# Kernel tuning notes

Measured on AMD Instinct MI355X. Metric: run time of the kernel, lower is better.

Reference implementation:

```python
import jax, jax.numpy as jnp
import numpy as np

NEG_SLOPE = 0.2  # LeakyReLU slope
B, F_BAND, T = 32, 128, 2048
HID, NCLASS = 256, 64


def _corrcoef(m):
    # m: [..., n, k] -> correlation matrix between rows, [..., n, n] (torch.corrcoef semantics)
    m = m - m.mean(axis=-1, keepdims=True)
    c = jnp.einsum('...ik,...jk->...ij', m, m)
    d = jnp.sqrt(jnp.clip(jnp.diagonal(c, axis1=-2, axis2=-1), 0.0, None))
    corr = c / (d[..., :, None] * d[..., None, :])
    return jnp.clip(corr, -1.0, 1.0)


def _leaky(x):
    return jnp.where(x >= 0, x, NEG_SLOPE * x)


def setup_inputs() -> dict:
    key = jax.random.key(0)
    ks = jax.random.split(key, 9)
    def lin(k, fin, fout):
        return jax.random.normal(k, (fin, fout), dtype=jnp.float32) / np.sqrt(fin)
    x = jax.random.normal(ks[0], (B, F_BAND, T), dtype=jnp.float32)
    return {
        'x': x,
        'W1': lin(ks[1], T, HID),      'b1': jnp.zeros((HID,), jnp.float32),
        'W2': lin(ks[2], HID, HID),    'b2': jnp.zeros((HID,), jnp.float32),
        'W3': lin(ks[3], HID, NCLASS), 'b3': jnp.zeros((NCLASS,), jnp.float32),
        'W4': lin(ks[4], NCLASS, NCLASS), 'b4': jnp.zeros((NCLASS,), jnp.float32),
    }


def reference(x, W1, b1, W2, b2, W3, b3, W4, b4):
    Bs, Fb, Tt = x.shape
    node = Fb
    step = node  # typeFeature=2 -> overlap=0
    A = len(range(0, Tt - node, step))  # number of time windows
    # windows: x[:, :, a*node:(a+1)*node] -> [B, A, F, node]
    xw = x[:, :, :A * node].reshape(Bs, Fb, A, node).transpose(0, 2, 1, 3)
    # torch.corrcoef(fi.T): rows = window-column index (node), variables over F bands
    adj = _corrcoef(jnp.swapaxes(xw, -1, -2))  # [B, A, node, node] == [B, A, F, F]
    adj = jnp.nan_to_num((adj + 1.0) * 0.5)
    # gnnBlock vectorized over all A windows (x broadcast along A). Dropout is eval-mode no-op.
    h = _leaky(jnp.einsum('banm,bmt->bant', adj, x) @ W1 + b1)    # [B,A,F,HID]
    h = _leaky(jnp.einsum('banm,bamh->banh', adj, h) @ W2 + b2)   # [B,A,F,HID]
    xa = _leaky(jnp.einsum('banm,bamh->banh', adj, h) @ W3 + b3)  # [B,A,F,C]
    # typeFeature==2 head: mean over nodes, corrcoef over windows, gc4
    xa = xa.mean(axis=2)         # [B, A, C]
    adj2 = _corrcoef(xa)         # [B, A, A]
    out = _leaky(jnp.einsum('bij,bjc->bic', adj2, xa) @ W4 + b4)  # [B, A, C]
    # max over dim=1; GradMultiply with grad_mul=1.0 is identity in fwd
    return out.max(axis=1)       # [B, C]
```

## Files before the change

### kernel.cpp

```cpp
#include <hip/hip_runtime.h>


typedef float f32x4 __attribute__((ext_vector_type(4)));
typedef __bf16 bf16x8 __attribute__((ext_vector_type(8)));
typedef unsigned short u16x8 __attribute__((ext_vector_type(8)));

__device__ inline unsigned short f2b(float f) {
  unsigned int u = __float_as_uint(f);
  unsigned int r = u + 0x7fffu + ((u >> 16) & 1u);
  return (unsigned short)(r >> 16);
}
__device__ inline float leaky(float v) { return v >= 0.f ? v : 0.2f * v; }

#define SWZ(k, r) ((k) ^ (((r) & 7) << 3))

__global__ __launch_bounds__(256) void k_prepw(const float* __restrict__ W1,
                                               const float* __restrict__ W2,
                                               const float* __restrict__ W3,
                                               unsigned short* __restrict__ W1T,
                                               unsigned short* __restrict__ W2T,
                                               unsigned short* __restrict__ W3T) {
  __shared__ float t[64][65];
  const int bid = blockIdx.x;
  const int tid = threadIdx.x;
  const float* src;
  unsigned short* dst;
  int K, N, k0, n0;
  if (bid < 128) {
    src = W1; dst = W1T; K = 2048; N = 256;
    k0 = (bid >> 2) * 64; n0 = (bid & 3) * 64;
  } else if (bid < 144) {
    src = W2; dst = W2T; K = 256; N = 256;
    int i = bid - 128; k0 = (i >> 2) * 64; n0 = (i & 3) * 64;
  } else {
    src = W3; dst = W3T; K = 256; N = 64;
    int i = bid - 144; k0 = i * 64; n0 = 0;
  }
#pragma unroll
  for (int it = 0; it < 16; ++it) {
    int e = tid + it * 256, r = e >> 6, c = e & 63;
    t[r][c] = src[(size_t)(k0 + r) * N + n0 + c];
  }
  __syncthreads();
#pragma unroll
  for (int it = 0; it < 16; ++it) {
    int e = tid + it * 256, rr = e >> 6, cc = e & 63;
    dst[(size_t)(n0 + rr) * K + k0 + cc] = f2b(t[cc][rr]);
  }
}

__global__ __launch_bounds__(512) void k_front(const float* __restrict__ x,
                                               const unsigned short* __restrict__ W1T,
                                               unsigned short* __restrict__ xT,
                                               unsigned short* __restrict__ XW1T) {
  __shared__ __align__(16) char ldsbuf[16896];
  const int bid = blockIdx.x;
  const int tid = threadIdx.x;
  if (bid >= 64) {
    float (*t)[65] = reinterpret_cast<float (*)[65]>(ldsbuf);
    int i = bid - 64;
    int b = i >> 6, rem = i & 63;
    int t0 = (rem >> 1) * 64, f0 = (rem & 1) * 64;
    const float* xb = x + ((size_t)b * 128 + f0) * 2048 + t0;
    int r = tid >> 3, c8 = (tid & 7) * 8;
    f32x4 v0 = *(const f32x4*)&xb[(size_t)r * 2048 + c8];
    f32x4 v1 = *(const f32x4*)&xb[(size_t)r * 2048 + c8 + 4];
    *(f32x4*)&t[r][c8] = v0;
    *(f32x4*)&t[r][c8 + 4] = v1;
    __syncthreads();
    u16x8 s;
#pragma unroll
    for (int q = 0; q < 8; ++q) s[q] = f2b(t[c8 + q][r]);
    *(u16x8*)&xT[((size_t)b * 2048 + t0 + r) * 128 + f0 + c8] = s;
  } else {
    unsigned short (*sX)[64 * 64] = reinterpret_cast<unsigned short (*)[64 * 64]>(ldsbuf);
    const int b = bid >> 1, f0 = (bid & 1) * 64;
    const int w = tid >> 6, lane = tid & 63;
    const int l15 = lane & 15, l4 = lane >> 4;
    const float* xb = x + ((size_t)b * 128 + f0) * 2048;
    const int fr = tid >> 3, k8 = (tid & 7) * 8;
    f32x4 xr0, xr1;
    f32x4 acc[2][4] = {};

    auto LOADX = [&](int kb) {
      xr0 = *(const f32x4*)&xb[(size_t)fr * 2048 + kb * 64 + k8];
      xr1 = *(const f32x4*)&xb[(size_t)fr * 2048 + kb * 64 + k8 + 4];
    };
    auto STOREX = [&](int buf) {
      u16x8 s;
#pragma unroll
      for (int q = 0; q < 8; ++q) s[q] = f2b(q < 4 ? xr0[q] : xr1[q - 4]);
      *(u16x8*)&sX[buf][fr * 64 + SWZ(k8, fr)] = s;
    };

    LOADX(0);
    STOREX(0);
    __syncthreads();
    for (int kb = 0; kb < 32; ++kb) {
      if (kb < 31) LOADX(kb + 1);
      const int buf = kb & 1;
#pragma unroll
      for (int ks = 0; ks < 2; ++ks) {
        bf16x8 af[2];
#pragma unroll
        for (int mt = 0; mt < 2; ++mt)
          af[mt] = *(const bf16x8*)&W1T[(size_t)(w * 32 + mt * 16 + l15) * 2048 + kb * 64 + ks * 32 + l4 * 8];
#pragma unroll
        for (int nt = 0; nt < 4; ++nt) {
          int br = nt * 16 + l15;
          bf16x8 bf = *(const bf16x8*)&sX[buf][br * 64 + SWZ(ks * 32 + l4 * 8, br)];
#pragma unroll
          for (int mt = 0; mt < 2; ++mt)
            acc[mt][nt] = __builtin_amdgcn_mfma_f32_16x16x32_bf16(af[mt], bf, acc[mt][nt], 0, 0, 0);
        }
      }
      if (kb < 31) {
        STOREX(buf ^ 1);
        __syncthreads();
      }
    }
#pragma unroll
    for (int mt = 0; mt < 2; ++mt)
#pragma unroll
      for (int nt = 0; nt < 4; ++nt)
#pragma unroll
        for (int r = 0; r < 4; ++r) {
          int p = w * 32 + mt * 16 + l4 * 4 + r;
          XW1T[((size_t)b * 256 + p) * 128 + f0 + nt * 16 + l15] = f2b(acc[mt][nt][r]);
        }
  }
}

__global__ __launch_bounds__(512) void k_chain(
    const unsigned short* __restrict__ xT, const unsigned short* __restrict__ XW1T,
    const unsigned short* __restrict__ W2T, const unsigned short* __restrict__ W3T,
    const float* __restrict__ b1g, const float* __restrict__ b2g,
    const float* __restrict__ b3g, float* __restrict__ gXa) {
  __shared__ __align__(16) unsigned short R0[128 * 128];
  __shared__ __align__(16) unsigned short R1[128 * 128];
  __shared__ float fS[256];

  const int tid = threadIdx.x;
  const int w = tid >> 6, lane = tid & 63;
  const int l15 = lane & 15, l4 = lane >> 4;
  const int ridx = (blockIdx.x & 7) * 60 + (blockIdx.x >> 3);
  const int b = ridx / 15, a = ridx % 15;
  const int m0 = w * 16;
  const unsigned short* XWb = XW1T + (size_t)b * 256 * 128;
  const float inv128 = 1.f / 128.f;

  const unsigned short* src = xT + ((size_t)b * 2048 + (size_t)a * 128) * 128;
#pragma unroll 1
  for (int it = 0; it < 4; ++it) {
    int tt = tid + it * 512;
    int j = tt >> 4, f8 = (tt & 15) * 8;
    *(u16x8*)&R1[j * 128 + SWZ(f8, j)] = *(const u16x8*)&src[j * 128 + f8];
  }
  __syncthreads();

  bf16x8 afw[4];
#pragma unroll
  for (int ks = 0; ks < 4; ++ks) {
    int ar = m0 + l15;
    afw[ks] = *(const bf16x8*)&R1[ar * 128 + SWZ(ks * 32 + l4 * 8, ar)];
  }
  bf16x8 ones;
#pragma unroll
  for (int q = 0; q < 8; ++q) ones[q] = (__bf16)1.0f;
  f32x4 sacc = {}, dacc = {};
#pragma unroll
  for (int ks = 0; ks < 4; ++ks) {
    sacc = __builtin_amdgcn_mfma_f32_16x16x32_bf16(afw[ks], ones, sacc, 0, 0, 0);
    dacc = __builtin_amdgcn_mfma_f32_16x16x32_bf16(afw[ks], afw[ks], dacc, 0, 0, 0);
  }
#pragma unroll
  for (int r = 0; r < 4; ++r) {
    if (l15 == 0) fS[m0 + l4 * 4 + r] = sacc[r];
    if (l15 == l4 * 4 + r)
      fS[128 + m0 + l4 * 4 + r] = dacc[r] - sacc[r] * sacc[r] * inv128;
  }
  __syncthreads();

  float div[4];
#pragma unroll
  for (int r = 0; r < 4; ++r) {
    float d = fS[128 + m0 + l4 * 4 + r];
    div[r] = d > 0.f ? __frsqrt_rn(d) : 0.f;
  }
#pragma unroll 1
  for (int nt = 0; nt < 8; ++nt) {
    int col = nt * 16 + l15;
    f32x4 c = {};
#pragma unroll
    for (int ks = 0; ks < 4; ++ks) {
      bf16x8 bf = *(const bf16x8*)&R1[col * 128 + SWZ(ks * 32 + l4 * 8, col)];
      c = __builtin_amdgcn_mfma_f32_16x16x32_bf16(afw[ks], bf, c, 0, 0, 0);
    }
    float fc = fS[col];
    float dc = fS[128 + col];
    float djv = dc > 0.f ? __frsqrt_rn(dc) : 0.f;
#pragma unroll
    for (int r = 0; r < 4; ++r) {
      float v = (c[r] - sacc[r] * fc * inv128) * div[r] * djv;
      v = fminf(1.f, fmaxf(-1.f, v));
      v = 0.5f * v + 0.5f;
      if (div[r] == 0.f || djv == 0.f) v = 0.f;
      int row = m0 + l4 * 4 + r;
      R0[row * 128 + SWZ(col, row)] = f2b(v);
    }
  }
  bf16x8 afj[4];
#pragma unroll
  for (int ks = 0; ks < 4; ++ks)
    afj[ks] = *(const bf16x8*)&R0[(m0 + l15) * 128 + SWZ(ks * 32 + l4 * 8, m0 + l15)];
  __syncthreads();

#pragma unroll 1
  for (int half = 0; half < 2; ++half) {
    unsigned short* Rd = half ? R0 : R1;
#pragma unroll 1
    for (int nt = 0; nt < 8; ++nt) {
      f32x4 acc = {};
      const unsigned short* Bp = &XWb[(size_t)(half * 128 + nt * 16 + l15) * 128 + l4 * 8];
#pragma unroll
      for (int ks = 0; ks < 4; ++ks) {
        bf16x8 bf = *(const bf16x8*)&Bp[ks * 32];
        acc = __builtin_amdgcn_mfma_f32_16x16x32_bf16(afj[ks], bf, acc, 0, 0, 0);
      }
      float bias = b1g[half * 128 + nt * 16 + l15];
#pragma unroll
      for (int r = 0; r < 4; ++r) {
        int row = m0 + l4 * 4 + r;
        Rd[row * 128 + SWZ(nt * 16 + l15, row)] = f2b(leaky(acc[r] + bias));
      }
    }
  }
  __syncthreads();

  f32x4 u2[2][8] = {};
  {
#pragma unroll
    for (int ks = 0; ks < 8; ++ks) {
      bf16x8 a0 = *(const bf16x8*)&W2T[(size_t)(w * 32 + l15) * 256 + ks * 32 + l4 * 8];
      bf16x8 a1 = *(const bf16x8*)&W2T[(size_t)(w * 32 + 16 + l15) * 256 + ks * 32 + l4 * 8];
      const unsigned short* Rs = (ks < 4) ? R1 : R0;
      int kk = (ks & 3) * 32 + l4 * 8;
#pragma unroll
      for (int nt = 0; nt < 8; ++nt) {
        int br = nt * 16 + l15;
        bf16x8 bf = *(const bf16x8*)&Rs[br * 128 + SWZ(kk, br)];
        u2[0][nt] = __builtin_amdgcn_mfma_f32_16x16x32_bf16(a0, bf, u2[0][nt], 0, 0, 0);
        u2[1][nt] = __builtin_amdgcn_mfma_f32_16x16x32_bf16(a1, bf, u2[1][nt], 0, 0, 0);
      }
    }
  }
  __syncthreads();

#pragma unroll
  for (int mt = 0; mt < 2; ++mt)
#pragma unroll
    for (int nt = 0; nt < 8; ++nt)
#pragma unroll
      for (int r = 0; r < 4; ++r) {
        int grow = w * 32 + mt * 16 + l4 * 4 + r;
        int col = nt * 16 + l15;
        unsigned short* Rd = (grow < 128) ? R0 : R1;
        int lr = grow & 127;
        Rd[lr * 128 + SWZ(col, lr)] = f2b(u2[mt][nt][r]);
      }
  __syncthreads();

  f32x4 h2acc[16];
#pragma unroll
  for (int nt = 0; nt < 16; ++nt) h2acc[nt] = f32x4{0.f, 0.f, 0.f, 0.f};
#pragma unroll
  for (int ks = 0; ks < 4; ++ks)
#pragma unroll
    for (int nt = 0; nt < 16; ++nt) {
      int brl = (nt & 7) * 16 + l15;
      const unsigned short* Rs = (nt < 8) ? R0 : R1;
      bf16x8 bf = *(const bf16x8*)&Rs[brl * 128 + SWZ(ks * 32 + l4 * 8, brl)];
      h2acc[nt] = __builtin_amdgcn_mfma_f32_16x16x32_bf16(afj[ks], bf, h2acc[nt], 0, 0, 0);
    }
  __syncthreads();

#pragma unroll
  for (int nt = 0; nt < 16; ++nt) {
    float bias = b2g[nt * 16 + l15];
#pragma unroll
    for (int r = 0; r < 4; ++r) {
      int row = m0 + l4 * 4 + r;
      int coll = (nt & 7) * 16 + l15;
      unsigned short* Rd = (nt < 8) ? R0 : R1;
      Rd[row * 128 + SWZ(coll, row)] = f2b(leaky(h2acc[nt][r] + bias));
    }
  }
  __syncthreads();

  f32x4 u3[4] = {};
  const int mrow = (w >> 1) * 16, ntb = (w & 1) * 4;
#pragma unroll
  for (int kh = 0; kh < 2; ++kh) {
    const unsigned short* Rs = kh ? R1 : R0;
#pragma unroll
    for (int ks = 0; ks < 4; ++ks) {
      bf16x8 a3 = *(const bf16x8*)&W3T[(size_t)(mrow + l15) * 256 + kh * 128 + ks * 32 + l4 * 8];
#pragma unroll
      for (int nti = 0; nti < 4; ++nti) {
        int br = (ntb + nti) * 16 + l15;
        bf16x8 bf = *(const bf16x8*)&Rs[br * 128 + SWZ(ks * 32 + l4 * 8, br)];
        u3[nti] = __builtin_amdgcn_mfma_f32_16x16x32_bf16(a3, bf, u3[nti], 0, 0, 0);
      }
    }
  }
  __syncthreads();

#pragma unroll
  for (int nti = 0; nti < 4; ++nti)
#pragma unroll
    for (int r = 0; r < 4; ++r) {
      int grow = mrow + l4 * 4 + r;
      int col = (ntb + nti) * 16 + l15;
      R0[grow * 128 + SWZ(col, grow)] = f2b(u3[nti][r]);
    }
  __syncthreads();

  {
    float* pf = reinterpret_cast<float*>(R1);
#pragma unroll 1
    for (int nt = 0; nt < 4; ++nt) {
      f32x4 acc = {};
      int br = nt * 16 + l15;
#pragma unroll
      for (int ks = 0; ks < 4; ++ks) {
        bf16x8 bf = *(const bf16x8*)&R0[br * 128 + SWZ(ks * 32 + l4 * 8, br)];
        acc = __builtin_amdgcn_mfma_f32_16x16x32_bf16(afj[ks], bf, acc, 0, 0, 0);
      }
      float bias = b3g[br];
      float v = 0.f;
#pragma unroll
      for (int r = 0; r < 4; ++r) v += leaky(acc[r] + bias);
      v += __shfl_xor(v, 16);
      v += __shfl_xor(v, 32);
      if (l4 == 0) pf[w * 64 + br] = v;
    }
  }
  __syncthreads();
  if (tid < 64) {
    const float* pf = reinterpret_cast<const float*>(R1);
    float s = 0.f;
#pragma unroll
    for (int gg = 0; gg < 8; ++gg) s += pf[gg * 64 + tid];
    gXa[((size_t)b * 15 + a) * 64 + tid] = s * (1.f / 128.f);
  }
}

__global__ __launch_bounds__(256) void k_head(const float* __restrict__ gXa,
                                              const float* __restrict__ W4,
                                              const float* __restrict__ b4,
                                              float* __restrict__ out) {
  __shared__ float xb[15 * 64];
  __shared__ float c2[15 * 16];
  __shared__ float mu[15];
  __shared__ float dinv[15];
  __shared__ float yy[15 * 64];
  __shared__ float zz[15 * 64];
  const int b = blockIdx.x;
  const int tid = threadIdx.x;
  for (int e = tid; e < 960; e += 256) xb[e] = gXa[(size_t)b * 960 + e];
  __syncthreads();
  if (tid < 15) {
    float s = 0.f;
    for (int c = 0; c < 64; ++c) s += xb[tid * 64 + c];
    mu[tid] = s * (1.f / 64.f);
  }
  __syncthreads();
  if (tid < 225) {
    int p = tid / 15, q = tid % 15;
    float s = 0.f;
    for (int c = 0; c < 64; ++c)
      s += (xb[p * 64 + c] - mu[p]) * (xb[q * 64 + c] - mu[q]);
    c2[p * 16 + q] = s;
  }
  __syncthreads();
  if (tid < 15) {
    float d = c2[tid * 16 + tid];
    dinv[tid] = d > 0.f ? (1.f / sqrtf(d)) : 0.f;
  }
  __syncthreads();
  if (tid < 225) {
    int p = tid / 15, q = tid % 15;
    float v = c2[p * 16 + q] * dinv[p] * dinv[q];
    v = fminf(1.f, fmaxf(-1.f, v));
    if (dinv[p] == 0.f || dinv[q] == 0.f) v = 0.f;
    c2[p * 16 + q] = v;
  }
  __syncthreads();
  for (int e = tid; e < 960; e += 256) {
    int p = e >> 6, c = e & 63;
    float s = 0.f;
    for (int q = 0; q < 15; ++q) s += c2[p * 16 + q] * xb[q * 64 + c];
    yy[e] = s;
  }
  __syncthreads();
  for (int e = tid; e < 960; e += 256) {
    int p = e >> 6, c = e & 63;
    float s = b4[c];
    for (int k = 0; k < 64; ++k) s += yy[p * 64 + k] * W4[k * 64 + c];
    zz[e] = leaky(s);
  }
  __syncthreads();
  if (tid < 64) {
    float m = -INFINITY;
    for (int p = 0; p < 15; ++p) m = fmaxf(m, zz[p * 64 + tid]);
    out[(size_t)b * 64 + tid] = m;
  }
}

extern "C" void kernel_launch(void* const* d_in, const int* in_sizes, int n_in,
                              void* d_out, int out_size, void* d_ws, size_t ws_size,
                              hipStream_t stream) {
  const float* x  = (const float*)d_in[0];
  const float* W1 = (const float*)d_in[1];
  const float* b1 = (const float*)d_in[2];
  const float* W2 = (const float*)d_in[3];
  const float* b2 = (const float*)d_in[4];
  const float* W3 = (const float*)d_in[5];
  const float* b3 = (const float*)d_in[6];
  const float* W4 = (const float*)d_in[7];
  const float* b4 = (const float*)d_in[8];
  float* out = (float*)d_out;

  char* ws = (char*)d_ws;
  unsigned short* xT   = (unsigned short*)ws;
  unsigned short* XW1T = (unsigned short*)(ws + 16777216);
  unsigned short* W1T  = (unsigned short*)(ws + 18874368);
  unsigned short* W2T  = (unsigned short*)(ws + 19922944);
  unsigned short* W3T  = (unsigned short*)(ws + 20054016);
  float* gXa           = (float*)(ws + 20086784);

  k_prepw<<<148, 256, 0, stream>>>(W1, W2, W3, W1T, W2T, W3T);
  k_front<<<2112, 512, 0, stream>>>(x, W1T, xT, XW1T);
  k_chain<<<480, 512, 0, stream>>>(xT, XW1T, W2T, W3T, b1, b2, b3, gXa);
  k_head<<<32, 256, 0, stream>>>(gXa, W4, b4, out);
}
```

Baseline: 131.3 us.

## Move x transpose into weight prep kernel, split XW1 GEMM, prefetch operands in chain

The x-to-bf16 transpose now runs inside the weight-prep kernel instead of sharing a launch with the x·W1 GEMM, and that GEMM becomes its own 64-block kernel. In k_chain, global loads of the XW1 B tiles, W2 A fragments and W3 fragments are software-prefetched one iteration ahead or hoisted before a barrier, to hide global memory latency. The split gives the 64 GEMM blocks a launch with no competition from the transpose blocks, but that launch underfills the GPU. The transpose now uses 256-thread blocks with smaller 4-element stores, and the prefetching adds register pressure.

Result: slower. 139.7 us (+6.4%).

```diff
diff --git a/kernel.cpp b/kernel.cpp
--- a/kernel.cpp
+++ b/kernel.cpp
@@ -3,6 +3,7 @@
 
 typedef float f32x4 __attribute__((ext_vector_type(4)));
 typedef __bf16 bf16x8 __attribute__((ext_vector_type(8)));
+typedef unsigned short u16x4 __attribute__((ext_vector_type(4)));
 typedef unsigned short u16x8 __attribute__((ext_vector_type(8)));
 
 __device__ inline unsigned short f2b(float f) {
@@ -14,121 +15,126 @@
 
 #define SWZ(k, r) ((k) ^ (((r) & 7) << 3))
 
-__global__ __launch_bounds__(256) void k_prepw(const float* __restrict__ W1,
-                                               const float* __restrict__ W2,
-                                               const float* __restrict__ W3,
-                                               unsigned short* __restrict__ W1T,
-                                               unsigned short* __restrict__ W2T,
-                                               unsigned short* __restrict__ W3T) {
+__global__ __launch_bounds__(256) void k_prep(const float* __restrict__ x,
+                                              const float* __restrict__ W1,
+                                              const float* __restrict__ W2,
+                                              const float* __restrict__ W3,
+                                              unsigned short* __restrict__ W1T,
+                                              unsigned short* __restrict__ W2T,
+                                              unsigned short* __restrict__ W3T,
+                                              unsigned short* __restrict__ xT) {
   __shared__ float t[64][65];
   const int bid = blockIdx.x;
   const int tid = threadIdx.x;
-  const float* src;
-  unsigned short* dst;
-  int K, N, k0, n0;
-  if (bid < 128) {
-    src = W1; dst = W1T; K = 2048; N = 256;
-    k0 = (bid >> 2) * 64; n0 = (bid & 3) * 64;
-  } else if (bid < 144) {
-    src = W2; dst = W2T; K = 256; N = 256;
-    int i = bid - 128; k0 = (i >> 2) * 64; n0 = (i & 3) * 64;
+  if (bid < 148) {
+    const float* src;
+    unsigned short* dst;
+    int K, N, k0, n0;
+    if (bid < 128) {
+      src = W1; dst = W1T; K = 2048; N = 256;
+      k0 = (bid >> 2) * 64; n0 = (bid & 3) * 64;
+    } else if (bid < 144) {
+      src = W2; dst = W2T; K = 256; N = 256;
+      int i = bid - 128; k0 = (i >> 2) * 64; n0 = (i & 3) * 64;
+    } else {
+      src = W3; dst = W3T; K = 256; N = 64;
+      int i = bid - 144; k0 = i * 64; n0 = 0;
+    }
+#pragma unroll
+    for (int it = 0; it < 16; ++it) {
+      int e = tid + it * 256, r = e >> 6, c = e & 63;
+      t[r][c] = src[(size_t)(k0 + r) * N + n0 + c];
+    }
+    __syncthreads();
+#pragma unroll
+    for (int it = 0; it < 16; ++it) {
+      int e = tid + it * 256, rr = e >> 6, cc = e & 63;
+      dst[(size_t)(n0 + rr) * K + k0 + cc] = f2b(t[cc][rr]);
+    }
   } else {
-    src = W3; dst = W3T; K = 256; N = 64;
-    int i = bid - 144; k0 = i * 64; n0 = 0;
-  }
-#pragma unroll
-  for (int it = 0; it < 16; ++it) {
-    int e = tid + it * 256, r = e >> 6, c = e & 63;
-    t[r][c] = src[(size_t)(k0 + r) * N + n0 + c];
-  }
-  __syncthreads();
-#pragma unroll
-  for (int it = 0; it < 16; ++it) {
-    int e = tid + it * 256, rr = e >> 6, cc = e & 63;
-    dst[(size_t)(n0 + rr) * K + k0 + cc] = f2b(t[cc][rr]);
-  }
-}
-
-__global__ __launch_bounds__(512) void k_front(const float* __restrict__ x,
-                                               const unsigned short* __restrict__ W1T,
-                                               unsigned short* __restrict__ xT,
-                                               unsigned short* __restrict__ XW1T) {
-  __shared__ __align__(16) char ldsbuf[16896];
+    int idx = bid - 148;
+    int b = idx >> 6, rem = idx & 63;
+    int tt = rem >> 1, ft = rem & 1;
+    int t0 = tt * 64, f0 = ft * 64;
+    const float* xb = x + ((size_t)b * 128 + f0) * 2048 + t0;
+#pragma unroll
+    for (int it = 0; it < 16; ++it) {
+      int e = tid + it * 256, r = e >> 6, c = e & 63;
+      t[r][c] = xb[(size_t)r * 2048 + c];
+    }
+    __syncthreads();
+    unsigned short* dst = xT + ((size_t)b * 2048 + t0) * 128 + f0;
+#pragma unroll
+    for (int it = 0; it < 4; ++it) {
+      int e = tid + it * 256, rr = e >> 4, c4 = (e & 15) * 4;
+      u16x4 s;
+#pragma unroll
+      for (int q = 0; q < 4; ++q) s[q] = f2b(t[c4 + q][rr]);
+      *(u16x4*)&dst[rr * 128 + c4] = s;
+    }
+  }
+}
+
+__global__ __launch_bounds__(512) void k_xw1(const float* __restrict__ x,
+                                             const unsigned short* __restrict__ W1T,
+                                             unsigned short* __restrict__ XW1T) {
+  __shared__ __align__(16) unsigned short sX[2][64 * 64];
   const int bid = blockIdx.x;
   const int tid = threadIdx.x;
-  if (bid >= 64) {
-    float (*t)[65] = reinterpret_cast<float (*)[65]>(ldsbuf);
-    int i = bid - 64;
-    int b = i >> 6, rem = i & 63;
-    int t0 = (rem >> 1) * 64, f0 = (rem & 1) * 64;
-    const float* xb = x + ((size_t)b * 128 + f0) * 2048 + t0;
-    int r = tid >> 3, c8 = (tid & 7) * 8;
-    f32x4 v0 = *(const f32x4*)&xb[(size_t)r * 2048 + c8];
-    f32x4 v1 = *(const f32x4*)&xb[(size_t)r * 2048 + c8 + 4];
-    *(f32x4*)&t[r][c8] = v0;
-    *(f32x4*)&t[r][c8 + 4] = v1;
-    __syncthreads();
+  const int b = bid >> 1, f0 = (bid & 1) * 64;
+  const int w = tid >> 6, lane = tid & 63;
+  const int l15 = lane & 15, l4 = lane >> 4;
+  const float* xb = x + ((size_t)b * 128 + f0) * 2048;
+  const int fr = tid >> 3, k8 = (tid & 7) * 8;
+  f32x4 xr0, xr1;
+  f32x4 acc[2][4] = {};
+
+  auto LOADX = [&](int kb) {
+    xr0 = *(const f32x4*)&xb[(size_t)fr * 2048 + kb * 64 + k8];
+    xr1 = *(const f32x4*)&xb[(size_t)fr * 2048 + kb * 64 + k8 + 4];
+  };
+  auto STOREX = [&](int buf) {
     u16x8 s;
 #pragma unroll
-    for (int q = 0; q < 8; ++q) s[q] = f2b(t[c8 + q][r]);
-    *(u16x8*)&xT[((size_t)b * 2048 + t0 + r) * 128 + f0 + c8] = s;
-  } else {
-    unsigned short (*sX)[64 * 64] = reinterpret_cast<unsigned short (*)[64 * 64]>(ldsbuf);
-    const int b = bid >> 1, f0 = (bid & 1) * 64;
-    const int w = tid >> 6, lane = tid & 63;
-    const int l15 = lane & 15, l4 = lane >> 4;
-    const float* xb = x + ((size_t)b * 128 + f0) * 2048;
-    const int fr = tid >> 3, k8 = (tid & 7) * 8;
-    f32x4 xr0, xr1;
-    f32x4 acc[2][4] = {};
-
-    auto LOADX = [&](int kb) {
-      xr0 = *(const f32x4*)&xb[(size_t)fr * 2048 + kb * 64 + k8];
-      xr1 = *(const f32x4*)&xb[(size_t)fr * 2048 + kb * 64 + k8 + 4];
-    };
-    auto STOREX = [&](int buf) {
-      u16x8 s;
-#pragma unroll
-      for (int q = 0; q < 8; ++q) s[q] = f2b(q < 4 ? xr0[q] : xr1[q - 4]);
-      *(u16x8*)&sX[buf][fr * 64 + SWZ(k8, fr)] = s;
-    };
-
-    LOADX(0);
-    STOREX(0);
-    __syncthreads();
-    for (int kb = 0; kb < 32; ++kb) {
-      if (kb < 31) LOADX(kb + 1);
-      const int buf = kb & 1;
-#pragma unroll
-      for (int ks = 0; ks < 2; ++ks) {
-        bf16x8 af[2];
+    for (int q = 0; q < 8; ++q) s[q] = f2b(q < 4 ? xr0[q] : xr1[q - 4]);
+    *(u16x8*)&sX[buf][fr * 64 + SWZ(k8, fr)] = s;
+  };
+
+  LOADX(0);
+  STOREX(0);
+  __syncthreads();
+  for (int kb = 0; kb < 32; ++kb) {
+    if (kb < 31) LOADX(kb + 1);
+    const int buf = kb & 1;
+#pragma unroll
+    for (int ks = 0; ks < 2; ++ks) {
+      bf16x8 af[2];
+#pragma unroll
+      for (int mt = 0; mt < 2; ++mt)
+        af[mt] = *(const bf16x8*)&W1T[(size_t)(w * 32 + mt * 16 + l15) * 2048 + kb * 64 + ks * 32 + l4 * 8];
+#pragma unroll
+      for (int nt = 0; nt < 4; ++nt) {
+        int br = nt * 16 + l15;
+        bf16x8 bf = *(const bf16x8*)&sX[buf][br * 64 + SWZ(ks * 32 + l4 * 8, br)];
 #pragma unroll
         for (int mt = 0; mt < 2; ++mt)
-          af[mt] = *(const bf16x8*)&W1T[(size_t)(w * 32 + mt * 16 + l15) * 2048 + kb * 64 + ks * 32 + l4 * 8];
-#pragma unroll
-        for (int nt = 0; nt < 4; ++nt) {
-          int br = nt * 16 + l15;
-          bf16x8 bf = *(const bf16x8*)&sX[buf][br * 64 + SWZ(ks * 32 + l4 * 8, br)];
-#pragma unroll
-          for (int mt = 0; mt < 2; ++mt)
-            acc[mt][nt] = __builtin_amdgcn_mfma_f32_16x16x32_bf16(af[mt], bf, acc[mt][nt], 0, 0, 0);
-        }
-      }
-      if (kb < 31) {
-        STOREX(buf ^ 1);
-        __syncthreads();
-      }
-    }
-#pragma unroll
-    for (int mt = 0; mt < 2; ++mt)
-#pragma unroll
-      for (int nt = 0; nt < 4; ++nt)
-#pragma unroll
-        for (int r = 0; r < 4; ++r) {
-          int p = w * 32 + mt * 16 + l4 * 4 + r;
-          XW1T[((size_t)b * 256 + p) * 128 + f0 + nt * 16 + l15] = f2b(acc[mt][nt][r]);
-        }
-  }
+          acc[mt][nt] = __builtin_amdgcn_mfma_f32_16x16x32_bf16(af[mt], bf, acc[mt][nt], 0, 0, 0);
+      }
+    }
+    if (kb < 31) {
+      STOREX(buf ^ 1);
+      __syncthreads();
+    }
+  }
+#pragma unroll
+  for (int mt = 0; mt < 2; ++mt)
+#pragma unroll
+    for (int nt = 0; nt < 4; ++nt)
+#pragma unroll
+      for (int r = 0; r < 4; ++r) {
+        int p = w * 32 + mt * 16 + l4 * 4 + r;
+        XW1T[((size_t)b * 256 + p) * 128 + f0 + nt * 16 + l15] = f2b(acc[mt][nt][r]);
+      }
 }
 
 __global__ __launch_bounds__(512) void k_chain(
@@ -218,15 +224,25 @@
 #pragma unroll 1
   for (int half = 0; half < 2; ++half) {
     unsigned short* Rd = half ? R0 : R1;
+    const unsigned short* Bbase = &XWb[(size_t)half * 128 * 128 + l4 * 8];
+    bf16x8 bpf[4];
+#pragma unroll
+    for (int ks = 0; ks < 4; ++ks)
+      bpf[ks] = *(const bf16x8*)&Bbase[(size_t)l15 * 128 + ks * 32];
 #pragma unroll 1
     for (int nt = 0; nt < 8; ++nt) {
+      bf16x8 bc[4];
+#pragma unroll
+      for (int ks = 0; ks < 4; ++ks) bc[ks] = bpf[ks];
+      if (nt < 7) {
+#pragma unroll
+        for (int ks = 0; ks < 4; ++ks)
+          bpf[ks] = *(const bf16x8*)&Bbase[(size_t)((nt + 1) * 16 + l15) * 128 + ks * 32];
+      }
       f32x4 acc = {};
-      const unsigned short* Bp = &XWb[(size_t)(half * 128 + nt * 16 + l15) * 128 + l4 * 8];
-#pragma unroll
-      for (int ks = 0; ks < 4; ++ks) {
-        bf16x8 bf = *(const bf16x8*)&Bp[ks * 32];
-        acc = __builtin_amdgcn_mfma_f32_16x16x32_bf16(afj[ks], bf, acc, 0, 0, 0);
-      }
+#pragma unroll
+      for (int ks = 0; ks < 4; ++ks)
+        acc = __builtin_amdgcn_mfma_f32_16x16x32_bf16(afj[ks], bc[ks], acc, 0, 0, 0);
       float bias = b1g[half * 128 + nt * 16 + l15];
 #pragma unroll
       for (int r = 0; r < 4; ++r) {
@@ -239,10 +255,17 @@
 
   f32x4 u2[2][8] = {};
   {
-#pragma unroll
+    const unsigned short* A0 = &W2T[(size_t)(w * 32 + l15) * 256 + l4 * 8];
+    const unsigned short* A1 = &W2T[(size_t)(w * 32 + 16 + l15) * 256 + l4 * 8];
+    bf16x8 a0p = *(const bf16x8*)&A0[0];
+    bf16x8 a1p = *(const bf16x8*)&A1[0];
+#pragma unroll 1
     for (int ks = 0; ks < 8; ++ks) {
-      bf16x8 a0 = *(const bf16x8*)&W2T[(size_t)(w * 32 + l15) * 256 + ks * 32 + l4 * 8];
-      bf16x8 a1 = *(const bf16x8*)&W2T[(size_t)(w * 32 + 16 + l15) * 256 + ks * 32 + l4 * 8];
+      bf16x8 a0 = a0p, a1 = a1p;
+      if (ks < 7) {
+        a0p = *(const bf16x8*)&A0[(ks + 1) * 32];
+        a1p = *(const bf16x8*)&A1[(ks + 1) * 32];
+      }
       const unsigned short* Rs = (ks < 4) ? R1 : R0;
       int kk = (ks & 3) * 32 + l4 * 8;
 #pragma unroll
@@ -295,21 +318,24 @@
       Rd[row * 128 + SWZ(coll, row)] = f2b(leaky(h2acc[nt][r] + bias));
     }
   }
+  const int mrow = (w >> 1) * 16, ntb = (w & 1) * 4;
+  bf16x8 a3f[8];
+#pragma unroll
+  for (int ks = 0; ks < 8; ++ks)
+    a3f[ks] = *(const bf16x8*)&W3T[(size_t)(mrow + l15) * 256 + ks * 32 + l4 * 8];
   __syncthreads();
 
   f32x4 u3[4] = {};
-  const int mrow = (w >> 1) * 16, ntb = (w & 1) * 4;
 #pragma unroll
   for (int kh = 0; kh < 2; ++kh) {
     const unsigned short* Rs = kh ? R1 : R0;
 #pragma unroll
     for (int ks = 0; ks < 4; ++ks) {
-      bf16x8 a3 = *(const bf16x8*)&W3T[(size_t)(mrow + l15) * 256 + kh * 128 + ks * 32 + l4 * 8];
 #pragma unroll
       for (int nti = 0; nti < 4; ++nti) {
         int br = (ntb + nti) * 16 + l15;
         bf16x8 bf = *(const bf16x8*)&Rs[br * 128 + SWZ(ks * 32 + l4 * 8, br)];
-        u3[nti] = __builtin_amdgcn_mfma_f32_16x16x32_bf16(a3, bf, u3[nti], 0, 0, 0);
+        u3[nti] = __builtin_amdgcn_mfma_f32_16x16x32_bf16(a3f[kh * 4 + ks], bf, u3[nti], 0, 0, 0);
       }
     }
   }
@@ -439,8 +465,8 @@
   unsigned short* W3T  = (unsigned short*)(ws + 20054016);
   float* gXa           = (float*)(ws + 20086784);
 
-  k_prepw<<<148, 256, 0, stream>>>(W1, W2, W3, W1T, W2T, W3T);
-  k_front<<<2112, 512, 0, stream>>>(x, W1T, xT, XW1T);
+  k_prep<<<2196, 256, 0, stream>>>(x, W1, W2, W3, W1T, W2T, W3T, xT);
+  k_xw1<<<64, 512, 0, stream>>>(x, W1T, XW1T);
   k_chain<<<480, 512, 0, stream>>>(xT, XW1T, W2T, W3T, b1, b2, b3, gXa);
   k_head<<<32, 256, 0, stream>>>(gXa, W4, b4, out);
 }
```
